# Optimization experiments

Measured on AMD Instinct MI355X. Metric: run time of the kernel, lower is better.

Reference implementation:

```python
import jax, jax.numpy as jnp
import numpy as np

# ---- constants from SystemsOfSprings.f ----
TS = 0.05                      # integration step h
K_G, C_G = 1.0, 2.0            # ground spring / damper (k1..k4, c1..c4)
K_I, C_I = 1.0, 0.0            # inter-agent spring / damper (k5..k10, c5..c10)
_L9 = float(np.sqrt(4.0 ** 2 + 1.5 ** 2))
EDGE_I = jnp.array([0, 1, 2, 3, 2, 3])          # springs 5,6,7,8,9,10
EDGE_J = jnp.array([1, 2, 3, 0, 0, 1])
EDGE_L = jnp.array([4.0, 1.5, 4.0, 1.5, _L9, _L9], dtype=jnp.float32)
XBAR = jnp.array([2.0, 2.0, 0.0, 0.0, -2.0, 2.0, 0.0, 0.0,
                  -2.0, -2.0, 0.0, 0.0, 2.0, -2.0, 0.0, 0.0], dtype=jnp.float32)


def _step(x, u, xbar):
    # x: (16,) = [px,py,vx,vy] x 4 agents; u: (8,) = 2 force inputs per agent
    px, py, vx, vy = x[0::4], x[1::4], x[2::4], x[3::4]      # (4,) each (Mx/My/Mvx/Mvy selections)
    xt, yt = xbar[0::4], xbar[1::4]

    # ground spring + damper forces (toward target, opposing velocity)
    dxt, dyt = px - xt, py - yt
    ang_t = jnp.arctan2(dyt, dxt)
    ang_v = jnp.arctan2(vy, vx)
    Fk0 = K_G * jnp.sqrt(dxt ** 2 + dyt ** 2)
    Fc0 = C_G * jnp.sqrt(vx ** 2 + vy ** 2)
    Fgx = -Fk0 * jnp.cos(ang_t) - Fc0 * jnp.cos(ang_v)
    Fgy = -Fk0 * jnp.sin(ang_t) - Fc0 * jnp.sin(ang_v)

    # inter-agent springs/dampers on the 6 edges (edge list, no 4x4 diagonal NaNs)
    dxe = px[EDGE_I] - px[EDGE_J]
    dye = py[EDGE_I] - py[EDGE_J]
    dvxe = vx[EDGE_I] - vx[EDGE_J]
    dvye = vy[EDGE_I] - vy[EDGE_J]
    Fke = K_I * (jnp.sqrt(dxe ** 2 + dye ** 2) - EDGE_L)
    Fce = C_I * jnp.sqrt(dvxe ** 2 + dvye ** 2)
    ang = jnp.arctan2(dye, dxe)      # angle from j toward i's perspective at i
    angv = jnp.arctan2(dvye, dvxe)
    cxe, sye = jnp.cos(ang), jnp.sin(ang)
    cve, sve = jnp.cos(angv), jnp.sin(angv)
    # force on agent i: -F*proj(i,j); on agent j: -F*proj(j,i) = +F*proj(i,j)
    z4 = jnp.zeros(4, x.dtype)
    Fsx = z4.at[EDGE_I].add(-Fke * cxe).at[EDGE_J].add(Fke * cxe)
    Fsy = z4.at[EDGE_I].add(-Fke * sye).at[EDGE_J].add(Fke * sye)
    Fdx = z4.at[EDGE_I].add(-Fce * cve).at[EDGE_J].add(Fce * cve)
    Fdy = z4.at[EDGE_I].add(-Fce * sve).at[EDGE_J].add(Fce * sve)

    accx = Fsx + Fdx + Fgx  # masses m1..m4 = 1
    accy = Fsy + Fdy + Fgy

    dx = jnp.zeros(16, x.dtype)
    dx = dx.at[0::4].set(vx).at[1::4].set(vy).at[2::4].set(accx).at[3::4].set(accy)
    Bu = jnp.zeros(16, x.dtype).at[2::4].set(u[0::2]).at[3::4].set(u[1::2])
    return x + (dx + Bu) * TS


def setup_inputs() -> dict:
    key = jax.random.key(0)
    kx, ku = jax.random.split(key)
    B = 1048576
    x = jax.random.normal(kx, (B, 16), dtype=jnp.float32)
    u = jax.random.normal(ku, (B, 8), dtype=jnp.float32)
    return {"t": 0, "x": x, "u": u, "w": jnp.zeros((16,), jnp.float32), "xbar": XBAR}


def reference(t, x, u, w, xbar):
    # t and w are unused, exactly as in the torch forward; batch via vmap
    return jax.vmap(lambda xi, ui: _step(xi, ui, xbar))(x, u)
```

## Files before the change

### kernel.cpp

```cpp
#include <hip/hip_runtime.h>
#include <math.h>


#define TS 0.05f

__global__ __launch_bounds__(256) void springs_step_kernel(
    const float* __restrict__ x,
    const float* __restrict__ u,
    float* __restrict__ out,
    int B)
{
    int i = blockIdx.x * blockDim.x + threadIdx.x;
    if (i >= B) return;

    const float4* x4 = reinterpret_cast<const float4*>(x) + (size_t)i * 4;
    const float4* u4 = reinterpret_cast<const float4*>(u) + (size_t)i * 2;
    float4*       o4 = reinterpret_cast<float4*>(out) + (size_t)i * 4;

    float4 n0 = x4[0];
    float4 n1 = x4[1];
    float4 n2 = x4[2];
    float4 n3 = x4[3];
    float4 ua = u4[0];
    float4 ub = u4[1];

    float px[4] = { n0.x, n1.x, n2.x, n3.x };
    float py[4] = { n0.y, n1.y, n2.y, n3.y };
    float vx[4] = { n0.z, n1.z, n2.z, n3.z };
    float vy[4] = { n0.w, n1.w, n2.w, n3.w };

    const float xt[4] = { 2.f, -2.f, -2.f,  2.f };
    const float yt[4] = { 2.f,  2.f, -2.f, -2.f };

    float ax[4], ay[4];
#pragma unroll
    for (int n = 0; n < 4; ++n) {
        ax[n] = -(px[n] - xt[n]) - 2.f * vx[n];
        ay[n] = -(py[n] - yt[n]) - 2.f * vy[n];
    }

    const int   EI[6] = { 0, 1, 2, 3, 2, 3 };
    const int   EJ[6] = { 1, 2, 3, 0, 0, 1 };
    const float L9 = 4.272001873f;
    const float EL[6] = { 4.f, 1.5f, 4.f, 1.5f, L9, L9 };

#pragma unroll
    for (int e = 0; e < 6; ++e) {
        float dx = px[EI[e]] - px[EJ[e]];
        float dy = py[EI[e]] - py[EJ[e]];
        float d2 = dx * dx + dy * dy;
        float r  = sqrtf(d2);
        float inv = (r > 0.f) ? (1.f / r) : 0.f;
        float c = (r > 0.f) ? (dx * inv) : 1.f;
        float s = dy * inv;
        float Fk = r - EL[e];
        float fx = Fk * c;
        float fy = Fk * s;
        ax[EI[e]] -= fx;
        ay[EI[e]] -= fy;
        ax[EJ[e]] += fx;
        ay[EJ[e]] += fy;
    }

    float uu[8] = { ua.x, ua.y, ua.z, ua.w, ub.x, ub.y, ub.z, ub.w };

    float4 r0, r1, r2, r3;
    r0.x = px[0] + TS * vx[0];
    r0.y = py[0] + TS * vy[0];
    r0.z = vx[0] + TS * (ax[0] + uu[0]);
    r0.w = vy[0] + TS * (ay[0] + uu[1]);

    r1.x = px[1] + TS * vx[1];
    r1.y = py[1] + TS * vy[1];
    r1.z = vx[1] + TS * (ax[1] + uu[2]);
    r1.w = vy[1] + TS * (ay[1] + uu[3]);

    r2.x = px[2] + TS * vx[2];
    r2.y = py[2] + TS * vy[2];
    r2.z = vx[2] + TS * (ax[2] + uu[4]);
    r2.w = vy[2] + TS * (ay[2] + uu[5]);

    r3.x = px[3] + TS * vx[3];
    r3.y = py[3] + TS * vy[3];
    r3.z = vx[3] + TS * (ax[3] + uu[6]);
    r3.w = vy[3] + TS * (ay[3] + uu[7]);

    o4[0] = r0;
    o4[1] = r1;
    o4[2] = r2;
    o4[3] = r3;
}

extern "C" void kernel_launch(void* const* d_in, const int* in_sizes, int n_in,
                              void* d_out, int out_size, void* d_ws, size_t ws_size,
                              hipStream_t stream) {
    const float* x = (const float*)d_in[1];
    const float* u = (const float*)d_in[2];
    float* out = (float*)d_out;

    int B = in_sizes[1] / 16;
    int block = 256;
    int grid = (B + block - 1) / block;
    springs_step_kernel<<<grid, block, 0, stream>>>(x, u, out, B);
}
```

Measured before the change: 153.4 us.

## Map one thread per agent node and exchange positions via wave shuffles

Each thread now handles one of the four agents in a batch item instead of the whole item. Neighbour positions come from __shfl_xor across lanes, and each thread computes its three spring forces directly. This makes the float4 loads and stores fully coalesced and raises the thread count fourfold, at the cost of computing each edge force twice. The kernel is memory-bound, so the main gain sought is better access patterns, not less arithmetic.

```diff
diff --git a/kernel.cpp b/kernel.cpp
--- a/kernel.cpp
+++ b/kernel.cpp
@@ -4,91 +4,57 @@
 
 #define TS 0.05f
 
-__global__ __launch_bounds__(256) void springs_step_kernel(
+__global__ __launch_bounds__(256) void springs_node_kernel(
     const float* __restrict__ x,
     const float* __restrict__ u,
     float* __restrict__ out,
-    int B)
+    int N)
 {
-    int i = blockIdx.x * blockDim.x + threadIdx.x;
-    if (i >= B) return;
+    int g = blockIdx.x * blockDim.x + threadIdx.x;
+    if (g >= N) return;
 
-    const float4* x4 = reinterpret_cast<const float4*>(x) + (size_t)i * 4;
-    const float4* u4 = reinterpret_cast<const float4*>(u) + (size_t)i * 2;
-    float4*       o4 = reinterpret_cast<float4*>(out) + (size_t)i * 4;
+    int node = g & 3;
 
-    float4 n0 = x4[0];
-    float4 n1 = x4[1];
-    float4 n2 = x4[2];
-    float4 n3 = x4[3];
-    float4 ua = u4[0];
-    float4 ub = u4[1];
+    float4 s  = reinterpret_cast<const float4*>(x)[g];
+    float2 uc = reinterpret_cast<const float2*>(u)[g];
 
-    float px[4] = { n0.x, n1.x, n2.x, n3.x };
-    float py[4] = { n0.y, n1.y, n2.y, n3.y };
-    float vx[4] = { n0.z, n1.z, n2.z, n3.z };
-    float vy[4] = { n0.w, n1.w, n2.w, n3.w };
+    float px = s.x, py = s.y, vx = s.z, vy = s.w;
 
-    const float xt[4] = { 2.f, -2.f, -2.f,  2.f };
-    const float yt[4] = { 2.f,  2.f, -2.f, -2.f };
+    float xt = (node == 1 || node == 2) ? -2.f : 2.f;
+    float yt = (node >= 2) ? -2.f : 2.f;
 
-    float ax[4], ay[4];
+    float ax = -(px - xt) - 2.f * vx;
+    float ay = -(py - yt) - 2.f * vy;
+
+    const float Ld[3] = { 4.0f, 4.2720018727f , 1.5f };
+
 #pragma unroll
-    for (int n = 0; n < 4; ++n) {
-        ax[n] = -(px[n] - xt[n]) - 2.f * vx[n];
-        ay[n] = -(py[n] - yt[n]) - 2.f * vy[n];
+    for (int d = 1; d <= 3; ++d) {
+        float qx = __shfl_xor(px, d, 64);
+        float qy = __shfl_xor(py, d, 64);
+        float dx = px - qx;
+        float dy = py - qy;
+        float d2 = dx * dx + dy * dy;
+        float L  = Ld[d - 1];
+
+        float r    = sqrtf(d2);
+        bool  nz   = (d2 > 0.f);
+        float invr = nz ? (1.f / r) : 0.f;
+        float c    = nz ? (dx * invr) : 1.f;
+        float sn   = dy * invr;
+        float Fk   = r - L;
+
+        ax -= Fk * c;
+        ay -= Fk * sn;
     }
 
-    const int   EI[6] = { 0, 1, 2, 3, 2, 3 };
-    const int   EJ[6] = { 1, 2, 3, 0, 0, 1 };
-    const float L9 = 4.272001873f;
-    const float EL[6] = { 4.f, 1.5f, 4.f, 1.5f, L9, L9 };
+    float4 r4;
+    r4.x = px + TS * vx;
+    r4.y = py + TS * vy;
+    r4.z = vx + TS * (ax + uc.x);
+    r4.w = vy + TS * (ay + uc.y);
 
-#pragma unroll
-    for (int e = 0; e < 6; ++e) {
-        float dx = px[EI[e]] - px[EJ[e]];
-        float dy = py[EI[e]] - py[EJ[e]];
-        float d2 = dx * dx + dy * dy;
-        float r  = sqrtf(d2);
-        float inv = (r > 0.f) ? (1.f / r) : 0.f;
-        float c = (r > 0.f) ? (dx * inv) : 1.f;
-        float s = dy * inv;
-        float Fk = r - EL[e];
-        float fx = Fk * c;
-        float fy = Fk * s;
-        ax[EI[e]] -= fx;
-        ay[EI[e]] -= fy;
-        ax[EJ[e]] += fx;
-        ay[EJ[e]] += fy;
-    }
-
-    float uu[8] = { ua.x, ua.y, ua.z, ua.w, ub.x, ub.y, ub.z, ub.w };
-
-    float4 r0, r1, r2, r3;
-    r0.x = px[0] + TS * vx[0];
-    r0.y = py[0] + TS * vy[0];
-    r0.z = vx[0] + TS * (ax[0] + uu[0]);
-    r0.w = vy[0] + TS * (ay[0] + uu[1]);
-
-    r1.x = px[1] + TS * vx[1];
-    r1.y = py[1] + TS * vy[1];
-    r1.z = vx[1] + TS * (ax[1] + uu[2]);
-    r1.w = vy[1] + TS * (ay[1] + uu[3]);
-
-    r2.x = px[2] + TS * vx[2];
-    r2.y = py[2] + TS * vy[2];
-    r2.z = vx[2] + TS * (ax[2] + uu[4]);
-    r2.w = vy[2] + TS * (ay[2] + uu[5]);
-
-    r3.x = px[3] + TS * vx[3];
-    r3.y = py[3] + TS * vy[3];
-    r3.z = vx[3] + TS * (ax[3] + uu[6]);
-    r3.w = vy[3] + TS * (ay[3] + uu[7]);
-
-    o4[0] = r0;
-    o4[1] = r1;
-    o4[2] = r2;
-    o4[3] = r3;
+    reinterpret_cast<float4*>(out)[g] = r4;
 }
 
 extern "C" void kernel_launch(void* const* d_in, const int* in_sizes, int n_in,
@@ -98,8 +64,8 @@
     const float* u = (const float*)d_in[2];
     float* out = (float*)d_out;
 
-    int B = in_sizes[1] / 16;
+    int N = in_sizes[1] / 4;
     int block = 256;
-    int grid = (B + block - 1) / block;
-    springs_step_kernel<<<grid, block, 0, stream>>>(x, u, out, B);
+    int grid = (N + block - 1) / block;
+    springs_node_kernel<<<grid, block, 0, stream>>>(x, u, out, N);
 }
```

After: 145.6 us. -5.1%, faster.
